# Optimization experiments

Hardware: AMD Instinct MI355X
Metric: run time of the kernel (lower is better)

Reference implementation:

```python
import jax, jax.numpy as jnp
import numpy as np

H = 16      # n_heads
D = 1024    # d_model
DK = D // H # head dim


def setup_inputs() -> dict:
    key = jax.random.key(0)
    ks = jax.random.split(key, 11)
    B, S = 4, 2048
    std = 1.0 / np.sqrt(D)
    inp = {
        "query": jax.random.normal(ks[0], (B, S, D), jnp.float32),
        "key": jax.random.normal(ks[1], (B, S, D), jnp.float32),
        "value": jax.random.normal(ks[2], (B, S, D), jnp.float32),
        "Wq": jax.random.normal(ks[3], (D, D), jnp.float32) * std,
        "bq": jnp.zeros((D,), jnp.float32),
        "Wk": jax.random.normal(ks[4], (D, D), jnp.float32) * std,
        "bk": jnp.zeros((D,), jnp.float32),
        "Wv": jax.random.normal(ks[5], (D, D), jnp.float32) * std,
        "bv": jnp.zeros((D,), jnp.float32),
        "Wo": jax.random.normal(ks[6], (D, D), jnp.float32) * std,
        "bo": jnp.zeros((D,), jnp.float32),
    }
    return inp


def reference(query, key, value, Wq, bq, Wk, bk, Wv, bv, Wo, bo):
    B, S, _ = query.shape
    # QKV projections (nn.Linear), then split heads: [B, S, H, DK]
    q = (query @ Wq + bq).reshape(B, S, H, DK)
    k = (key @ Wk + bk).reshape(B, S, H, DK)
    v = (value @ Wv + bv).reshape(B, S, H, DK)
    # Memory-efficient attention computes exactly softmax(QK^T/sqrt(dk))V
    scale = 1.0 / np.sqrt(DK).astype(np.float32)
    scores = jnp.einsum("bqhd,bkhd->bhqk", q, k) * scale  # [B, H, S, S]
    attn = jax.nn.softmax(scores, axis=-1)
    x = jnp.einsum("bhqk,bkhd->bqhd", attn, v)            # [B, S, H, DK]
    x = x.reshape(B, S, H * DK)
    return x @ Wo + bo
```

## Files before the change

kernel.cpp:

```cpp
#include <hip/hip_runtime.h>
#include <hip/hip_bf16.h>

typedef short short8 __attribute__((ext_vector_type(8)));
typedef float f32x4 __attribute__((ext_vector_type(4)));
typedef float f32x16 __attribute__((ext_vector_type(16)));
typedef unsigned short u16;
typedef unsigned int u32;

#define HD 16
#define DMODEL 1024
#define DKH 64
#define SEQ 2048
#define QSCALE 0.18033688f

typedef const __attribute__((address_space(1))) void gvoid;
typedef __attribute__((address_space(3))) void lvoid;

__device__ inline u16 f2bf(float f) {
  unsigned int x = __builtin_bit_cast(unsigned int, f);
  unsigned int r = (x + 0x7fffu + ((x >> 16) & 1u)) >> 16;
  return (u16)r;
}

__device__ inline float fexp2(float x) {
#if __has_builtin(__builtin_amdgcn_exp2f)
  return __builtin_amdgcn_exp2f(x);
#else
  return __expf(x * 0.69314718f);
#endif
}

__device__ inline u32 cvtpk(float lo, float hi_) {
  u32 r;
  asm("v_cvt_pk_bf16_f32 %0, %1, %2" : "=v"(r) : "v"(lo), "v"(hi_));
  return r;
}

__device__ inline void pswap(u32& a, u32& b) {
  asm volatile("v_permlane32_swap_b32 %0, %1" : "+v"(a), "+v"(b));
}

__device__ inline f32x4 mfma16(short8 a, short8 b, f32x4 c) {
  return __builtin_amdgcn_mfma_f32_16x16x32_bf16(a, b, c, 0, 0, 0);
}
__device__ inline f32x16 mfma32(short8 a, short8 b, f32x16 c) {
  return __builtin_amdgcn_mfma_f32_32x32x16_bf16(a, b, c, 0, 0, 0);
}

__global__ __launch_bounds__(256) void prep_kernel(const float* __restrict__ q,
                                                   const float* __restrict__ k,
                                                   const float* __restrict__ v,
                                                   const float* __restrict__ W0,
                                                   const float* __restrict__ W1,
                                                   const float* __restrict__ W2,
                                                   const float* __restrict__ W3,
                                                   u16* __restrict__ Qf,
                                                   u16* __restrict__ Kf,
                                                   u16* __restrict__ Vf,
                                                   u16* __restrict__ WT) {
  const int z = blockIdx.z;
  if (z < 3) {
    const float* src = z == 0 ? q : z == 1 ? k : v;
    u16* dst = z == 0 ? Qf : z == 1 ? Kf : Vf;
    const int nthr = gridDim.x * 256;
    for (size_t i = blockIdx.x * 256 + threadIdx.x; i < (size_t)(SEQ * 4) * DMODEL / 8; i += nthr) {
      const float4 a0 = *(const float4*)(src + i * 8);
      const float4 a1 = *(const float4*)(src + i * 8 + 4);
      u32 tmp[4] = {cvtpk(a0.x, a0.y), cvtpk(a0.z, a0.w),
                    cvtpk(a1.x, a1.y), cvtpk(a1.z, a1.w)};
      *(uint4*)(dst + i * 8) = *(uint4*)tmp;
    }
  } else {
    __shared__ float tile[64][65];
    const int b = blockIdx.x;
    const int w = b >> 8;
    const int n0 = (b & 15) * 64, k0 = ((b >> 4) & 15) * 64;
    const float* W = w == 0 ? W0 : w == 1 ? W1 : w == 2 ? W2 : W3;
    u16* out = WT + (size_t)w * DMODEL * DMODEL;
    int tx = threadIdx.x & 63, ty = threadIdx.x >> 6;
    for (int i = 0; i < 16; i++) {
      int r = ty + i * 4;
      tile[r][tx] = W[(size_t)(k0 + r) * DMODEL + n0 + tx];
    }
    __syncthreads();
    for (int i = 0; i < 16; i++) {
      int r = ty + i * 4;
      out[(size_t)(n0 + r) * DMODEL + k0 + tx] = f2bf(tile[tx][r]);
    }
  }
}

__global__ __launch_bounds__(256, 2) void gemm_qkv(const u16* __restrict__ Qf,
                                                   const u16* __restrict__ Kf,
                                                   const u16* __restrict__ Vf,
                                                   const u16* __restrict__ WT,
                                                   const float* __restrict__ bq,
                                                   const float* __restrict__ bk,
                                                   const float* __restrict__ bv,
                                                   u16* __restrict__ Qb,
                                                   u16* __restrict__ Kb,
                                                   u16* __restrict__ Vtb) {
  __shared__ u16 As[2][128 * 64];
  __shared__ u16 Bs[2][128 * 64];
  const int b = blockIdx.x;
  const int xcd = b & 7, slot = b >> 3;
  const int nidx = slot & 7, pl = slot >> 3;
  const int pg = xcd * 24 + pl;
  const int z = pg >> 6, by = pg & 63;

  const u16* A = z == 0 ? Qf : z == 1 ? Kf : Vf;
  const u16* Bt = WT + (size_t)z * DMODEL * DMODEL;
  const float* bias = z == 0 ? bq : z == 1 ? bk : bv;
  u16* Cv = z == 0 ? Qb : z == 1 ? Kb : Vtb;
  const float scale = z == 0 ? QSCALE : 1.0f;
  const bool vtrans = (z == 2);

  const int m0 = by * 128, n0 = nidx * 128;
  const int tid = threadIdx.x;
  const int lane = tid & 63, wid = tid >> 6;
  const int g = lane >> 4, c = lane & 15;
  const int wr = (wid >> 1) * 64, wc = (wid & 1) * 64;

  const int trow = tid >> 3;
  const int tcolb = (tid & 7) << 4;
  const int swr = (c & 7) << 4;
  f32x4 acc[4][4] = {};

#define STAGE_AB(buf, kk0)                                                            \
  _Pragma("unroll") for (int p = 0; p < 4; ++p) {                                     \
    const int row = p * 32 + trow;                                                    \
    const int scol = tcolb ^ ((row & 7) << 4);                                        \
    __builtin_amdgcn_global_load_lds(                                                 \
        (gvoid*)((const char*)A + ((size_t)(m0 + row) * DMODEL + (kk0)) * 2 + scol),  \
        (lvoid*)((char*)&As[buf][0] + row * 128 + tcolb), 16, 0, 0);                  \
    __builtin_amdgcn_global_load_lds(                                                 \
        (gvoid*)((const char*)Bt + ((size_t)(n0 + row) * DMODEL + (kk0)) * 2 + scol), \
        (lvoid*)((char*)&Bs[buf][0] + row * 128 + tcolb), 16, 0, 0);                  \
  }

  STAGE_AB(0, 0);
  STAGE_AB(1, 64);
  __syncthreads();

  for (int t = 0; t < 16; ++t) {
    const int cur = t & 1;
    short8 af[4][2], bfr[4][2];
#pragma unroll
    for (int kk = 0; kk < 2; ++kk) {
#pragma unroll
      for (int mi = 0; mi < 4; ++mi)
        af[mi][kk] = *(const short8*)((const char*)&As[cur][0] + (wr + mi * 16 + c) * 128 + ((kk * 64 + g * 16) ^ swr));
#pragma unroll
      for (int ni = 0; ni < 4; ++ni)
        bfr[ni][kk] = *(const short8*)((const char*)&Bs[cur][0] + (wc + ni * 16 + c) * 128 + ((kk * 64 + g * 16) ^ swr));
    }
    __builtin_amdgcn_s_setprio(1);
#pragma unroll
    for (int kk = 0; kk < 2; ++kk)
#pragma unroll
      for (int mi = 0; mi < 4; ++mi)
#pragma unroll
        for (int ni = 0; ni < 4; ++ni)
          acc[mi][ni] = mfma16(af[mi][kk], bfr[ni][kk], acc[mi][ni]);
    __builtin_amdgcn_s_setprio(0);
    __syncthreads();
    if (t < 14) STAGE_AB(cur, (t + 2) * 64);
  }
#undef STAGE_AB

  for (int ni = 0; ni < 4; ++ni) {
    const int colg = n0 + wc + ni * 16 + c;
    const float bv_ = bias[colg];
    for (int mi = 0; mi < 4; ++mi) {
      const int rowb = m0 + wr + mi * 16 + g * 4;
      const int bb = rowb >> 11, s = rowb & 2047;
      const int h = colg >> 6, dk = colg & 63;
      if (!vtrans) {
        const size_t base = ((size_t)(bb * HD + h)) * SEQ;
        for (int j = 0; j < 4; ++j)
          Cv[(base + s + j) * DKH + dk] = f2bf((acc[mi][ni][j] + bv_) * scale);
      } else {
        const size_t base = ((size_t)(bb * HD + h) * DKH + dk) * SEQ + s;
        ushort4 u;
        u.x = f2bf(acc[mi][ni][0] + bv_);
        u.y = f2bf(acc[mi][ni][1] + bv_);
        u.z = f2bf(acc[mi][ni][2] + bv_);
        u.w = f2bf(acc[mi][ni][3] + bv_);
        *(ushort4*)(&Cv[base]) = u;
      }
    }
  }
}

__global__ __launch_bounds__(256, 2) void gemm_out(const u16* __restrict__ A,
                                                   const u16* __restrict__ Bt,
                                                   const float* __restrict__ bias,
                                                   float* __restrict__ C) {
  __shared__ u16 As[2][128 * 64];
  __shared__ u16 Bs[2][128 * 64];
  const int b = blockIdx.x;
  const int xcd = b & 7, slot = b >> 3;
  const int nidx = slot & 7, pl = slot >> 3;
  const int by = xcd * 8 + pl;

  const int m0 = by * 128, n0 = nidx * 128;
  const int tid = threadIdx.x;
  const int lane = tid & 63, wid = tid >> 6;
  const int g = lane >> 4, c = lane & 15;
  const int wr = (wid >> 1) * 64, wc = (wid & 1) * 64;

  const int trow = tid >> 3;
  const int tcolb = (tid & 7) << 4;
  const int swr = (c & 7) << 4;
  f32x4 acc[4][4] = {};

#define STAGE_AB(buf, kk0)                                                            \
  _Pragma("unroll") for (int p = 0; p < 4; ++p) {                                     \
    const int row = p * 32 + trow;                                                    \
    const int scol = tcolb ^ ((row & 7) << 4);                                        \
    __builtin_amdgcn_global_load_lds(                                                 \
        (gvoid*)((const char*)A + ((size_t)(m0 + row) * DMODEL + (kk0)) * 2 + scol),  \
        (lvoid*)((char*)&As[buf][0] + row * 128 + tcolb), 16, 0, 0);                  \
    __builtin_amdgcn_global_load_lds(                                                 \
        (gvoid*)((const char*)Bt + ((size_t)(n0 + row) * DMODEL + (kk0)) * 2 + scol), \
        (lvoid*)((char*)&Bs[buf][0] + row * 128 + tcolb), 16, 0, 0);                  \
  }

  STAGE_AB(0, 0);
  STAGE_AB(1, 64);
  __syncthreads();

  for (int t = 0; t < 16; ++t) {
    const int cur = t & 1;
    short8 af[4][2], bfr[4][2];
#pragma unroll
    for (int kk = 0; kk < 2; ++kk) {
#pragma unroll
      for (int mi = 0; mi < 4; ++mi)
        af[mi][kk] = *(const short8*)((const char*)&As[cur][0] + (wr + mi * 16 + c) * 128 + ((kk * 64 + g * 16) ^ swr));
#pragma unroll
      for (int ni = 0; ni < 4; ++ni)
        bfr[ni][kk] = *(const short8*)((const char*)&Bs[cur][0] + (wc + ni * 16 + c) * 128 + ((kk * 64 + g * 16) ^ swr));
    }
    __builtin_amdgcn_s_setprio(1);
#pragma unroll
    for (int kk = 0; kk < 2; ++kk)
#pragma unroll
      for (int mi = 0; mi < 4; ++mi)
#pragma unroll
        for (int ni = 0; ni < 4; ++ni)
          acc[mi][ni] = mfma16(af[mi][kk], bfr[ni][kk], acc[mi][ni]);
    __builtin_amdgcn_s_setprio(0);
    __syncthreads();
    if (t < 14) STAGE_AB(cur, (t + 2) * 64);
  }
#undef STAGE_AB

  for (int ni = 0; ni < 4; ++ni) {
    const int colg = n0 + wc + ni * 16 + c;
    const float bv = bias[colg];
    for (int mi = 0; mi < 4; ++mi) {
      const int rowb = m0 + wr + mi * 16 + g * 4;
      for (int j = 0; j < 4; ++j)
        C[(size_t)(rowb + j) * DMODEL + colg] = acc[mi][ni][j] + bv;
    }
  }
}

__global__ __launch_bounds__(256, 4) void attn_kernel(const u16* __restrict__ Q,
                                                      const u16* __restrict__ K,
                                                      const u16* __restrict__ Vt,
                                                      u16* __restrict__ X) {
  __shared__ char Kls[2][8192];
  __shared__ char Vls[3][8192];
  const int tid = threadIdx.x;
  const int lane = tid & 63, wid = tid >> 6;
  const int c5 = lane & 31, hi = lane >> 5;

  const int blk = blockIdx.x;
  const int work = (blk & 7) * 128 + (blk >> 3);
  const int qt = work & 15, bh = work >> 4;

  const int q0 = qt * 128 + wid * 32;
  const u16* qb = Q + (size_t)bh * SEQ * DKH;
  const char* kbB = (const char*)(K + (size_t)bh * SEQ * DKH);
  const char* vbB = (const char*)(Vt + (size_t)bh * DKH * SEQ);

  short8 qf[4];
#pragma unroll
  for (int ks = 0; ks < 4; ++ks)
    qf[ks] = *(const short8*)(qb + (size_t)(q0 + c5) * DKH + ks * 16 + hi * 8);

  const int srow = tid >> 3;
  const int scolb = (tid & 7) << 4;
  const int scol = scolb ^ ((srow & 7) << 4);

  const int fswz = (c5 & 7) << 4;
  int cofs[4];
#pragma unroll
  for (int ks = 0; ks < 4; ++ks) cofs[ks] = ((ks * 32 + hi * 16) ^ fswz);

  f32x16 oacc[2] = {};
  f32x16 sacc[2];
  float lrun = 0.f;

#define STAGE_K(t, dst)                                                         \
  _Pragma("unroll") for (int r32 = 0; r32 < 64; r32 += 32)                      \
      __builtin_amdgcn_global_load_lds(                                         \
          (gvoid*)(kbB + ((size_t)(t) * 64 + r32 + srow) * 128 + scol),         \
          (lvoid*)((dst) + (r32 + srow) * 128 + scolb), 16, 0, 0);
#define STAGE_V(t, dst)                                                         \
  _Pragma("unroll") for (int r32 = 0; r32 < 64; r32 += 32)                      \
      __builtin_amdgcn_global_load_lds(                                         \
          (gvoid*)(vbB + (size_t)(r32 + srow) * (SEQ * 2) + (size_t)(t) * 128 + scol), \
          (lvoid*)((dst) + (r32 + srow) * 128 + scolb), 16, 0, 0);
#define QKT(bufK)                                                               \
  _Pragma("unroll") for (int kt = 0; kt < 2; ++kt) {                            \
    short8 kf[4];                                                               \
    _Pragma("unroll") for (int ks = 0; ks < 4; ++ks)                            \
        kf[ks] = *(const short8*)((bufK) + (kt * 32 + c5) * 128 + cofs[ks]);    \
    sacc[kt] = (f32x16){};                                                      \
    _Pragma("unroll") for (int ks = 0; ks < 4; ++ks)                            \
        sacc[kt] = mfma32(kf[ks], qf[ks], sacc[kt]);                            \
  }

  STAGE_K(0, Kls[0]); STAGE_V(0, Vls[0]);
  STAGE_K(1, Kls[1]); STAGE_V(1, Vls[1]);
  __syncthreads();
  QKT(Kls[0]);
  __syncthreads();

  char* pk_nxt = Kls[1];
  char* pk_stg = Kls[0];
  char* pv_cur = Vls[0];
  char* pv_nxt = Vls[1];
  char* pv_stg = Vls[2];

  for (int t = 0; t < 32; ++t) {
    if (t < 30) {
      STAGE_K(t + 2, pk_stg);
      STAGE_V(t + 2, pv_stg);
    }

    float rs = 0.f;
    u32 W[2][8];
#pragma unroll
    for (int kt = 0; kt < 2; ++kt)
#pragma unroll
      for (int j = 0; j < 8; ++j) {
        float p0 = fexp2(sacc[kt][2 * j]);
        float p1 = fexp2(sacc[kt][2 * j + 1]);
        rs += p0 + p1;
        W[kt][j] = cvtpk(p0, p1);
      }
    rs += __shfl_xor(rs, 32, 64);
    lrun += rs;

    short8 pa[4];
#pragma unroll
    for (int ks = 0; ks < 4; ++ks) {
      const int kt = ks >> 1, l4 = (ks & 1) * 4;
      u32 a0 = W[kt][l4 + 0], b0 = W[kt][l4 + 2];
      u32 a1 = W[kt][l4 + 1], b1 = W[kt][l4 + 3];
      pswap(a0, b0);
      pswap(a1, b1);
      u32 tmp[4] = {a0, a1, b0, b1};
      pa[ks] = *(const short8*)tmp;
    }

    if (t < 31) {
      __builtin_amdgcn_s_setprio(1);
      QKT(pk_nxt);
      __builtin_amdgcn_s_setprio(0);
    }

    __builtin_amdgcn_s_setprio(1);
#pragma unroll
    for (int ks = 0; ks < 4; ++ks)
#pragma unroll
      for (int dkt = 0; dkt < 2; ++dkt) {
        short8 vf = *(const short8*)(pv_cur + (dkt * 32 + c5) * 128 + cofs[ks]);
        oacc[dkt] = mfma32(pa[ks], vf, oacc[dkt]);
      }
    __builtin_amdgcn_s_setprio(0);

    __syncthreads();

    char* tk = pk_nxt; pk_nxt = pk_stg; pk_stg = tk;
    char* tv = pv_cur; pv_cur = pv_nxt; pv_nxt = pv_stg; pv_stg = tv;
  }

#undef QKT
#undef STAGE_K
#undef STAGE_V

  const int b = bh >> 4, h = bh & 15;
  const float inv = 1.0f / lrun;
#pragma unroll
  for (int r = 0; r < 16; ++r) {
    const int qrow = (r & 3) + 8 * (r >> 2) + 4 * hi;
    const float linv = __shfl(inv, qrow, 64);
    const size_t rowbase = ((size_t)(b * SEQ) + q0 + qrow) * DMODEL + h * DKH;
#pragma unroll
    for (int dkt = 0; dkt < 2; ++dkt)
      X[rowbase + dkt * 32 + c5] = f2bf(oacc[dkt][r] * linv);
  }
}

extern "C" void kernel_launch(void* const* d_in, const int* in_sizes, int n_in,
                              void* d_out, int out_size, void* d_ws, size_t ws_size,
                              hipStream_t stream) {
  (void)in_sizes; (void)n_in; (void)out_size; (void)ws_size;
  const float* query = (const float*)d_in[0];
  const float* key   = (const float*)d_in[1];
  const float* value = (const float*)d_in[2];
  const float* Wq = (const float*)d_in[3];
  const float* bq = (const float*)d_in[4];
  const float* Wk = (const float*)d_in[5];
  const float* bk = (const float*)d_in[6];
  const float* Wv = (const float*)d_in[7];
  const float* bv = (const float*)d_in[8];
  const float* Wo = (const float*)d_in[9];
  const float* bo = (const float*)d_in[10];
  float* out = (float*)d_out;

  char* ws = (char*)d_ws;
  const size_t MB = 1024 * 1024;
  u16* WT  = (u16*)ws;
  u16* Qf  = (u16*)(ws + 8 * MB);
  u16* Kf  = (u16*)(ws + 24 * MB);
  u16* Vf  = (u16*)(ws + 40 * MB);
  u16* Qb  = (u16*)(ws + 56 * MB);
  u16* Kb  = (u16*)(ws + 72 * MB);
  u16* Vtb = (u16*)(ws + 88 * MB);
  u16* Xb  = (u16*)(ws + 8 * MB);

  prep_kernel<<<dim3(1024, 1, 4), 256, 0, stream>>>(query, key, value, Wq, Wk, Wv, Wo,
                                                    Qf, Kf, Vf, WT);
  gemm_qkv<<<dim3(1536), 256, 0, stream>>>(Qf, Kf, Vf, WT, bq, bk, bv, Qb, Kb, Vtb);
  attn_kernel<<<dim3(1024), 256, 0, stream>>>(Qb, Kb, Vtb, Xb);
  gemm_out<<<dim3(512), 256, 0, stream>>>(Xb, WT + 3 * 1048576, bo, out);
}
```

Baseline: 190.0 us.

## Simplify attention pipeline to double buffering and compute row sums via MFMA

Replaces the software-pipelined loop, which computed the next tile's QK^T ahead of time and used triple-buffered V, with a plain double-buffered loop that computes QK^T and PV for the same tile. The softmax denominator is now accumulated with an extra MFMA against a vector of bf16 ones instead of scalar adds plus a cross-lane shuffle. This lowers LDS use and VALU work, but loses the overlap of QK^T MFMAs with the exp/convert step, and the row sums now come from bf16-rounded probabilities.

```diff
diff --git a/kernel.cpp b/kernel.cpp
--- a/kernel.cpp
+++ b/kernel.cpp
@@ -272,7 +272,7 @@
                                                       const u16* __restrict__ Vt,
                                                       u16* __restrict__ X) {
   __shared__ char Kls[2][8192];
-  __shared__ char Vls[3][8192];
+  __shared__ char Vls[2][8192];
   const int tid = threadIdx.x;
   const int lane = tid & 63, wid = tid >> 6;
   const int c5 = lane & 31, hi = lane >> 5;
@@ -291,6 +291,13 @@
   for (int ks = 0; ks < 4; ++ks)
     qf[ks] = *(const short8*)(qb + (size_t)(q0 + c5) * DKH + ks * 16 + hi * 8);
 
+  short8 onesf;
+  {
+    u32 o2 = 0x3F803F80u;
+    u32 arr[4] = {o2, o2, o2, o2};
+    onesf = *(const short8*)arr;
+  }
+
   const int srow = tid >> 3;
   const int scolb = (tid & 7) << 4;
   const int scol = scolb ^ ((srow & 7) << 4);
@@ -301,8 +308,7 @@
   for (int ks = 0; ks < 4; ++ks) cofs[ks] = ((ks * 32 + hi * 16) ^ fswz);
 
   f32x16 oacc[2] = {};
-  f32x16 sacc[2];
-  float lrun = 0.f;
+  f32x16 lacc = {};
 
 #define STAGE_K(t, dst)                                                         \
   _Pragma("unroll") for (int r32 = 0; r32 < 64; r32 += 32)                      \
@@ -314,47 +320,43 @@
       __builtin_amdgcn_global_load_lds(                                         \
           (gvoid*)(vbB + (size_t)(r32 + srow) * (SEQ * 2) + (size_t)(t) * 128 + scol), \
           (lvoid*)((dst) + (r32 + srow) * 128 + scolb), 16, 0, 0);
-#define QKT(bufK)                                                               \
-  _Pragma("unroll") for (int kt = 0; kt < 2; ++kt) {                            \
-    short8 kf[4];                                                               \
-    _Pragma("unroll") for (int ks = 0; ks < 4; ++ks)                            \
-        kf[ks] = *(const short8*)((bufK) + (kt * 32 + c5) * 128 + cofs[ks]);    \
-    sacc[kt] = (f32x16){};                                                      \
-    _Pragma("unroll") for (int ks = 0; ks < 4; ++ks)                            \
-        sacc[kt] = mfma32(kf[ks], qf[ks], sacc[kt]);                            \
-  }
-
-  STAGE_K(0, Kls[0]); STAGE_V(0, Vls[0]);
-  STAGE_K(1, Kls[1]); STAGE_V(1, Vls[1]);
+
+  STAGE_K(0, Kls[0]);
+  STAGE_V(0, Vls[0]);
   __syncthreads();
-  QKT(Kls[0]);
-  __syncthreads();
-
-  char* pk_nxt = Kls[1];
-  char* pk_stg = Kls[0];
-  char* pv_cur = Vls[0];
-  char* pv_nxt = Vls[1];
-  char* pv_stg = Vls[2];
-
+
+#pragma unroll 2
   for (int t = 0; t < 32; ++t) {
-    if (t < 30) {
-      STAGE_K(t + 2, pk_stg);
-      STAGE_V(t + 2, pv_stg);
-    }
-
-    float rs = 0.f;
+    const int buf = t & 1;
+    if (t < 31) {
+      STAGE_K(t + 1, Kls[buf ^ 1]);
+      STAGE_V(t + 1, Vls[buf ^ 1]);
+    }
+
+    const char* bK = Kls[buf];
+    const char* bV = Vls[buf];
+
+    f32x16 sacc[2];
+    __builtin_amdgcn_s_setprio(1);
+#pragma unroll
+    for (int kt = 0; kt < 2; ++kt) {
+      short8 kf[4];
+#pragma unroll
+      for (int ks = 0; ks < 4; ++ks)
+        kf[ks] = *(const short8*)(bK + (kt * 32 + c5) * 128 + cofs[ks]);
+      sacc[kt] = (f32x16){};
+#pragma unroll
+      for (int ks = 0; ks < 4; ++ks)
+        sacc[kt] = mfma32(kf[ks], qf[ks], sacc[kt]);
+    }
+    __builtin_amdgcn_s_setprio(0);
+
     u32 W[2][8];
 #pragma unroll
     for (int kt = 0; kt < 2; ++kt)
 #pragma unroll
-      for (int j = 0; j < 8; ++j) {
-        float p0 = fexp2(sacc[kt][2 * j]);
-        float p1 = fexp2(sacc[kt][2 * j + 1]);
-        rs += p0 + p1;
-        W[kt][j] = cvtpk(p0, p1);
-      }
-    rs += __shfl_xor(rs, 32, 64);
-    lrun += rs;
+      for (int j = 0; j < 8; ++j)
+        W[kt][j] = cvtpk(fexp2(sacc[kt][2 * j]), fexp2(sacc[kt][2 * j + 1]));
 
     short8 pa[4];
 #pragma unroll
@@ -368,38 +370,29 @@
       pa[ks] = *(const short8*)tmp;
     }
 
-    if (t < 31) {
-      __builtin_amdgcn_s_setprio(1);
-      QKT(pk_nxt);
-      __builtin_amdgcn_s_setprio(0);
-    }
-
     __builtin_amdgcn_s_setprio(1);
 #pragma unroll
-    for (int ks = 0; ks < 4; ++ks)
+    for (int ks = 0; ks < 4; ++ks) {
 #pragma unroll
       for (int dkt = 0; dkt < 2; ++dkt) {
-        short8 vf = *(const short8*)(pv_cur + (dkt * 32 + c5) * 128 + cofs[ks]);
+        short8 vf = *(const short8*)(bV + (dkt * 32 + c5) * 128 + cofs[ks]);
         oacc[dkt] = mfma32(pa[ks], vf, oacc[dkt]);
       }
+      lacc = mfma32(pa[ks], onesf, lacc);
+    }
     __builtin_amdgcn_s_setprio(0);
 
     __syncthreads();
-
-    char* tk = pk_nxt; pk_nxt = pk_stg; pk_stg = tk;
-    char* tv = pv_cur; pv_cur = pv_nxt; pv_nxt = pv_stg; pv_stg = tv;
-  }
-
-#undef QKT
+  }
+
 #undef STAGE_K
 #undef STAGE_V
 
   const int b = bh >> 4, h = bh & 15;
-  const float inv = 1.0f / lrun;
 #pragma unroll
   for (int r = 0; r < 16; ++r) {
     const int qrow = (r & 3) + 8 * (r >> 2) + 4 * hi;
-    const float linv = __shfl(inv, qrow, 64);
+    const float linv = 1.0f / lacc[r];
     const size_t rowbase = ((size_t)(b * SEQ) + q0 + qrow) * DMODEL + h * DKH;
 #pragma unroll
     for (int dkt = 0; dkt < 2; ++dkt)
```

After: 190.7 us. About the same (+0.3%).
